# Kernel tuning notes

Hardware: AMD Instinct MI355X
Metric: run time of the kernel (lower is better)

The kernel has to match this reference:

```python
import jax, jax.numpy as jnp
import numpy as np

N_NODES = 100000
N_EDGES = 1600000
IN_DIM, HID_DIM, OUT_DIM = 128, 64, 64


def _graph_conv(src, dst, h, W, b, n_nodes):
    # DGL GraphConv, norm='both': out = D_in^{-1/2} A (D_out^{-1/2} h W) + b
    ones = jnp.ones(src.shape[0], dtype=h.dtype)
    deg_out = jax.ops.segment_sum(ones, src, num_segments=n_nodes)
    deg_in = jax.ops.segment_sum(ones, dst, num_segments=n_nodes)
    norm_src = jax.lax.rsqrt(jnp.maximum(deg_out, 1.0))  # [N]
    norm_dst = jax.lax.rsqrt(jnp.maximum(deg_in, 1.0))   # [N]
    # project first (in_dim >= out_dim path), then aggregate over edges
    x = (h * norm_src[:, None]) @ W                      # [N, d_out]
    msg = x[src]                                         # [E, d_out] gather
    agg = jax.ops.segment_sum(msg, dst, num_segments=n_nodes)  # [N, d_out]
    return agg * norm_dst[:, None] + b


def setup_inputs() -> dict:
    key = jax.random.key(0)
    k = jax.random.split(key, 6)
    h = jax.random.normal(k[0], (N_NODES, IN_DIM), dtype=jnp.float32)
    src = jax.random.randint(k[1], (N_EDGES,), 0, N_NODES, dtype=jnp.int32)
    dst = jax.random.randint(k[2], (N_EDGES,), 0, N_NODES, dtype=jnp.int32)
    W1 = jax.random.normal(k[3], (IN_DIM, HID_DIM), dtype=jnp.float32) / np.sqrt(IN_DIM)
    b1 = jnp.zeros((HID_DIM,), dtype=jnp.float32)
    W2 = jax.random.normal(k[4], (HID_DIM, OUT_DIM), dtype=jnp.float32) / np.sqrt(HID_DIM)
    b2 = jnp.zeros((OUT_DIM,), dtype=jnp.float32)
    return {"h": h, "src": src, "dst": dst, "W1": W1, "b1": b1, "W2": W2, "b2": b2}


def reference(h, src, dst, W1, b1, W2, b2):
    x = _graph_conv(src, dst, h, W1, b1, N_NODES)
    x = jax.nn.elu(x)  # act = nn.ELU()
    x = _graph_conv(src, dst, x, W2, b2, N_NODES)
    return x  # last_act is None
```

## Files before the change

### kernel.cpp

```cpp
#include <hip/hip_runtime.h>
#include <math.h>

#define CH 4096
#define NBUK_MAX 256
#define MAXB 12288
#define SRC_BITS 17

typedef short bf16x8 __attribute__((ext_vector_type(8)));
typedef float f32x4 __attribute__((ext_vector_type(4)));
typedef float f32x2 __attribute__((ext_vector_type(2)));

__device__ __forceinline__ unsigned short f2bf(float f) {
    union { float f; unsigned int u; } v; v.f = f;
    unsigned int r = (v.u + 0x7FFFu + ((v.u >> 16) & 1u)) >> 16;
    return (unsigned short)r;
}
__device__ __forceinline__ float bf2f(unsigned short u) {
    union { unsigned int u; float f; } v; v.u = ((unsigned int)u) << 16;
    return v.f;
}
__device__ __forceinline__ float bflo(unsigned int u) {
    union { unsigned int u; float f; } v; v.u = u << 16;
    return v.f;
}
__device__ __forceinline__ float bfhi(unsigned int u) {
    union { unsigned int u; float f; } v; v.u = u & 0xFFFF0000u;
    return v.f;
}

__global__ __launch_bounds__(256) void p1a_kernel(const int* __restrict__ src, const int* __restrict__ dst,
                                                  int* __restrict__ mat, int E, int B1, int nbuk) {
    __shared__ int hd[NBUK_MAX], hs[NBUK_MAX];
    const int t = threadIdx.x;
    if (t < nbuk) { hd[t] = 0; hs[t] = 0; }
    __syncthreads();
    const int base = blockIdx.x * CH;
    const int cnt = min(CH, E - base);
    for (int k = t; k < cnt; k += 256) {
        int d = dst[base + k];
        int s = src[base + k];
        atomicAdd(&hd[d >> 9], 1);
        atomicAdd(&hs[s >> 9], 1);
    }
    __syncthreads();
    if (t < nbuk) {
        mat[t * B1 + blockIdx.x] = hd[t];
        mat[(nbuk + t) * B1 + blockIdx.x] = hs[t];
    }
}

__global__ __launch_bounds__(256) void scan1_kernel(const int* __restrict__ cnt,
                                                    int* __restrict__ seg,
                                                    int* __restrict__ bsums, int N) {
    __shared__ int tsum[256];
    const int t = threadIdx.x;
    const int base = blockIdx.x * 1024 + t * 4;
    int v0 = (base + 0 < N) ? cnt[base + 0] : 0;
    int v1 = (base + 1 < N) ? cnt[base + 1] : 0;
    int v2 = (base + 2 < N) ? cnt[base + 2] : 0;
    int v3 = (base + 3 < N) ? cnt[base + 3] : 0;
    tsum[t] = v0 + v1 + v2 + v3;
    __syncthreads();
    for (int off = 1; off < 256; off <<= 1) {
        int x = (t >= off) ? tsum[t - off] : 0;
        __syncthreads();
        if (t >= off) tsum[t] += x;
        __syncthreads();
    }
    int run = (t > 0) ? tsum[t - 1] : 0;
    if (base + 0 < N) seg[base + 0] = run; run += v0;
    if (base + 1 < N) seg[base + 1] = run; run += v1;
    if (base + 2 < N) seg[base + 2] = run; run += v2;
    if (base + 3 < N) seg[base + 3] = run;
    if (t == 255) bsums[blockIdx.x] = tsum[255];
}

__global__ void scan2_kernel(int* __restrict__ bsums, int* __restrict__ seg, int N, int G) {
    __shared__ int s[256];
    int t = threadIdx.x;
    if (t < G) s[t] = bsums[t];
    __syncthreads();
    if (t == 0) {
        int run = 0;
        for (int i = 0; i < G; ++i) { int v = s[i]; s[i] = run; run += v; }
        seg[N] = run;
    }
    __syncthreads();
    if (t < G) bsums[t] = s[t];
}

__global__ __launch_bounds__(256) void scan3_kernel(int* __restrict__ seg,
                                                    const int* __restrict__ bsums, int N) {
    int add = bsums[blockIdx.x];
    int base = blockIdx.x * 1024 + threadIdx.x * 4;
#pragma unroll
    for (int i = 0; i < 4; ++i) {
        int idx = base + i;
        if (idx < N) seg[idx] += add;
    }
}

__global__ __launch_bounds__(256) void p1c_kernel(const int* __restrict__ src, const int* __restrict__ dst,
                                                  const int* __restrict__ mat,
                                                  const int* __restrict__ scan,
                                                  int* __restrict__ pedge,
                                                  int E, int B1, int nbuk) {
    __shared__ int hd[NBUK_MAX], hs[NBUK_MAX];
    __shared__ int curD[NBUK_MAX], curS[NBUK_MAX];
    __shared__ int baseD[NBUK_MAX], baseS[NBUK_MAX];
    __shared__ int stD[CH];
    __shared__ int stS[CH];
    const int t = threadIdx.x;
    if (t < nbuk) {
        hd[t] = mat[t * B1 + blockIdx.x];
        hs[t] = mat[(nbuk + t) * B1 + blockIdx.x];
    }
    const int base = blockIdx.x * CH;
    const int cnt = min(CH, E - base);
    int dl[CH / 256], sl[CH / 256];
#pragma unroll
    for (int k = 0; k < CH / 256; ++k) {
        int i = t + k * 256;
        if (i < cnt) {
            dl[k] = dst[base + i];
            sl[k] = src[base + i];
        }
    }
    __syncthreads();
    for (int off = 1; off < nbuk; off <<= 1) {
        int v0 = (t >= off && t < nbuk) ? hd[t - off] : 0;
        int w0 = (t >= off && t < nbuk) ? hs[t - off] : 0;
        __syncthreads();
        if (t < nbuk) { hd[t] += v0; hs[t] += w0; }
        __syncthreads();
    }
    if (t < nbuk) {
        int excD = t ? hd[t - 1] : 0;
        int excS = t ? hs[t - 1] : 0;
        curD[t] = excD;
        curS[t] = excS;
        baseD[t] = scan[t * B1 + blockIdx.x] - excD;
        baseS[t] = scan[(nbuk + t) * B1 + blockIdx.x] - excS;
    }
    __syncthreads();
#pragma unroll
    for (int k = 0; k < CH / 256; ++k) {
        int i = t + k * 256;
        if (i < cnt) {
            int j = dl[k] >> 9;
            int p = atomicAdd(&curD[j], 1);
            stD[p] = ((dl[k] & 511) << SRC_BITS) | sl[k];
            int jq = sl[k] >> 9;
            int q = atomicAdd(&curS[jq], 1);
            stS[q] = sl[k];
        }
    }
    __syncthreads();
    for (int i = t; i < cnt; i += 256) {
        int lo = 0, hi = nbuk - 1;
        while (lo < hi) { int mid = (lo + hi) >> 1; if (hd[mid] > i) hi = mid; else lo = mid + 1; }
        pedge[baseD[lo] + i] = stD[i];
        int lo2 = 0, hi2 = nbuk - 1;
        while (lo2 < hi2) { int mid = (lo2 + hi2) >> 1; if (hs[mid] > i) hi2 = mid; else lo2 = mid + 1; }
        pedge[baseS[lo2] + i] = stS[i];
    }
}

__global__ __launch_bounds__(512) void p2s2_kernel(const int* __restrict__ pedge,
                                                   const int* __restrict__ scan,
                                                   int* __restrict__ esrc, int* __restrict__ seg,
                                                   float* __restrict__ norm_dst,
                                                   float* __restrict__ norm_src,
                                                   int N, int E, int B1, int nbuk) {
    __shared__ int h[512];
    __shared__ int cur[512];
    __shared__ int stage[MAXB];
    const int t = threadIdx.x;
    const int b0 = blockIdx.x;
    if (b0 >= nbuk) {
        const int b = b0 - nbuk;
        h[t] = 0;
        __syncthreads();
        const int sb0 = scan[(nbuk + b) * B1];
        const int sb1 = scan[(nbuk + b + 1) * B1];
        for (int i = sb0 + t; i < sb1; i += 512) atomicAdd(&h[pedge[i] & 511], 1);
        __syncthreads();
        int n = (b << 9) + t;
        if (n < N) norm_src[n] = rsqrtf(fmaxf((float)h[t], 1.0f));
        return;
    }
    const int b = b0;
    h[t] = 0;
    __syncthreads();
    const int bb0 = scan[b * B1];
    const int bb1 = scan[(b + 1) * B1];
    for (int i = bb0 + t; i < bb1; i += 512) atomicAdd(&h[(pedge[i] >> SRC_BITS) & 511], 1);
    __syncthreads();
    for (int off = 1; off < 512; off <<= 1) {
        int v = (t >= off) ? h[t - off] : 0;
        __syncthreads();
        h[t] += v;
        __syncthreads();
    }
    {
        int exc = t ? h[t - 1] : 0;
        cur[t] = exc;
        int n = (b << 9) + t;
        if (n < N) {
            seg[n] = bb0 + exc;
            norm_dst[n] = rsqrtf(fmaxf((float)(h[t] - exc), 1.0f));
        }
        if (b == 0 && t == 0) seg[N] = E;
    }
    __syncthreads();
    const int cnt = bb1 - bb0;
    for (int i = bb0 + t; i < bb1; i += 512) {
        int v = pedge[i];
        int j = (v >> SRC_BITS) & 511;
        int p = atomicAdd(&cur[j], 1);
        int s = v & ((1 << SRC_BITS) - 1);
        if (p < MAXB) stage[p] = s; else esrc[bb0 + p] = s;
    }
    __syncthreads();
    for (int i = t; i < cnt && i < MAXB; i += 512) esrc[bb0 + i] = stage[i];
}

template<int K>
__global__ __launch_bounds__(256) void gemm_norm(const float* __restrict__ H,
                                                 const float* __restrict__ W,
                                                 const float* __restrict__ norm,
                                                 unsigned short* __restrict__ X, int N) {
    constexpr int KP = K + 8;
    __shared__ __align__(16) unsigned short sHi[64 * KP];
    __shared__ __align__(16) unsigned short sLo[64 * KP];
    const int tid = threadIdx.x;

    for (int idx = tid; idx < K * 64; idx += 256) {
        int k = idx >> 6;
        int c = idx & 63;
        float v = W[idx];
        unsigned short hi = f2bf(v);
        sHi[c * KP + k] = hi;
        sLo[c * KP + k] = f2bf(v - bf2f(hi));
    }
    __syncthreads();

    const int w = tid >> 6;
    const int lane = tid & 63;
    const int quad = lane >> 4;
    const int l16 = lane & 15;
    const int n0 = blockIdx.x * 64;
    const int arow = n0 + w * 16 + l16;
    const int arow_c = (arow < N) ? arow : (N - 1);
    const float* Hrow = H + (size_t)arow_c * K + quad * 8;

    f32x4 acc[4];
#pragma unroll
    for (int t = 0; t < 4; ++t) acc[t] = (f32x4){0.0f, 0.0f, 0.0f, 0.0f};

    float4 p0 = *(const float4*)(Hrow + 0);
    float4 p1 = *(const float4*)(Hrow + 4);

#pragma unroll
    for (int kc = 0; kc < K / 32; ++kc) {
        const float v[8] = {p0.x, p0.y, p0.z, p0.w, p1.x, p1.y, p1.z, p1.w};
        bf16x8 aHi, aLo;
#pragma unroll
        for (int j = 0; j < 8; ++j) {
            unsigned short hi = f2bf(v[j]);
            aHi[j] = (short)hi;
            aLo[j] = (short)f2bf(v[j] - bf2f(hi));
        }
        if (kc + 1 < K / 32) {
            p0 = *(const float4*)(Hrow + (kc + 1) * 32 + 0);
            p1 = *(const float4*)(Hrow + (kc + 1) * 32 + 4);
        }
        const int kbase = kc * 32 + quad * 8;
#pragma unroll
        for (int t = 0; t < 4; ++t) {
            const int col = t * 16 + l16;
            const bf16x8 bHi = *(const bf16x8*)&sHi[col * KP + kbase];
            const bf16x8 bLo = *(const bf16x8*)&sLo[col * KP + kbase];
            acc[t] = __builtin_amdgcn_mfma_f32_16x16x32_bf16(aLo, bHi, acc[t], 0, 0, 0);
            acc[t] = __builtin_amdgcn_mfma_f32_16x16x32_bf16(aHi, bLo, acc[t], 0, 0, 0);
            acc[t] = __builtin_amdgcn_mfma_f32_16x16x32_bf16(aHi, bHi, acc[t], 0, 0, 0);
        }
    }

#pragma unroll
    for (int r = 0; r < 4; ++r) {
        const int node = n0 + w * 16 + quad * 4 + r;
        if (node < N) {
            const float s = norm[node];
#pragma unroll
            for (int t = 0; t < 4; ++t) {
                X[(size_t)node * 64 + t * 16 + l16] = f2bf(acc[t][r] * s);
            }
        } else if (node == N) {
#pragma unroll
            for (int t = 0; t < 4; ++t) {
                X[(size_t)node * 64 + t * 16 + l16] = 0;
            }
        }
    }
}

template<bool ELU>
__global__ __launch_bounds__(256) void segsum_kernel(const unsigned short* __restrict__ X,
                                                     const int* __restrict__ esrc,
                                                     const int* __restrict__ seg,
                                                     const float* __restrict__ norm_dst,
                                                     const float* __restrict__ bias,
                                                     float* __restrict__ out, int N) {
    const int node = blockIdx.x * 4 + (threadIdx.x >> 6);
    const int lane = threadIdx.x & 63;
    if (node >= N) return;
    const int eh = lane >> 4;
    const int fl = lane & 15;
    const int s0 = seg[node];
    const int s1 = seg[node + 1];
    const unsigned short* Xf = X + fl * 4;
    f32x2 A0 = {0.0f, 0.0f};
    f32x2 A1 = {0.0f, 0.0f};
    int e = s0;
    for (; e + 16 <= s1; e += 16) {
        const int base = e + eh * 4;
        const int r0 = esrc[base + 0];
        const int r1 = esrc[base + 1];
        const int r2 = esrc[base + 2];
        const int r3 = esrc[base + 3];
        const uint2 u0 = *(const uint2*)&Xf[(size_t)r0 * 64];
        const uint2 u1 = *(const uint2*)&Xf[(size_t)r1 * 64];
        const uint2 u2 = *(const uint2*)&Xf[(size_t)r2 * 64];
        const uint2 u3 = *(const uint2*)&Xf[(size_t)r3 * 64];
        A0 += (f32x2){bflo(u0.x), bfhi(u0.x)}; A1 += (f32x2){bflo(u0.y), bfhi(u0.y)};
        A0 += (f32x2){bflo(u1.x), bfhi(u1.x)}; A1 += (f32x2){bflo(u1.y), bfhi(u1.y)};
        A0 += (f32x2){bflo(u2.x), bfhi(u2.x)}; A1 += (f32x2){bflo(u2.y), bfhi(u2.y)};
        A0 += (f32x2){bflo(u3.x), bfhi(u3.x)}; A1 += (f32x2){bflo(u3.y), bfhi(u3.y)};
    }
    if (e < s1) {
        const int base = e + eh * 4;
        const int i0 = esrc[base + 0];
        const int i1 = esrc[base + 1];
        const int i2 = esrc[base + 2];
        const int i3 = esrc[base + 3];
        const int r0 = (base + 0 < s1) ? i0 : N;
        const int r1 = (base + 1 < s1) ? i1 : N;
        const int r2 = (base + 2 < s1) ? i2 : N;
        const int r3 = (base + 3 < s1) ? i3 : N;
        const uint2 u0 = *(const uint2*)&Xf[(size_t)r0 * 64];
        const uint2 u1 = *(const uint2*)&Xf[(size_t)r1 * 64];
        const uint2 u2 = *(const uint2*)&Xf[(size_t)r2 * 64];
        const uint2 u3 = *(const uint2*)&Xf[(size_t)r3 * 64];
        A0 += (f32x2){bflo(u0.x), bfhi(u0.x)}; A1 += (f32x2){bflo(u0.y), bfhi(u0.y)};
        A0 += (f32x2){bflo(u1.x), bfhi(u1.x)}; A1 += (f32x2){bflo(u1.y), bfhi(u1.y)};
        A0 += (f32x2){bflo(u2.x), bfhi(u2.x)}; A1 += (f32x2){bflo(u2.y), bfhi(u2.y)};
        A0 += (f32x2){bflo(u3.x), bfhi(u3.x)}; A1 += (f32x2){bflo(u3.y), bfhi(u3.y)};
    }
    float a0 = A0.x, a1 = A0.y, a2 = A1.x, a3 = A1.y;
    a0 += __shfl(a0, lane ^ 16); a1 += __shfl(a1, lane ^ 16);
    a2 += __shfl(a2, lane ^ 16); a3 += __shfl(a3, lane ^ 16);
    a0 += __shfl(a0, lane ^ 32); a1 += __shfl(a1, lane ^ 32);
    a2 += __shfl(a2, lane ^ 32); a3 += __shfl(a3, lane ^ 32);
    if (eh == 0) {
        const float s = norm_dst[node];
        const float4 bb = *(const float4*)&bias[fl * 4];
        float4 r;
        r.x = a0 * s + bb.x;
        r.y = a1 * s + bb.y;
        r.z = a2 * s + bb.z;
        r.w = a3 * s + bb.w;
        if (ELU) {
            r.x = r.x > 0.0f ? r.x : expm1f(r.x);
            r.y = r.y > 0.0f ? r.y : expm1f(r.y);
            r.z = r.z > 0.0f ? r.z : expm1f(r.z);
            r.w = r.w > 0.0f ? r.w : expm1f(r.w);
        }
        *(float4*)&out[(size_t)node * 64 + fl * 4] = r;
    }
}

extern "C" void kernel_launch(void* const* d_in, const int* in_sizes, int n_in,
                              void* d_out, int out_size, void* d_ws, size_t ws_size,
                              hipStream_t stream) {
    const float* h   = (const float*)d_in[0];
    const int*   src = (const int*)d_in[1];
    const int*   dst = (const int*)d_in[2];
    const float* W1  = (const float*)d_in[3];
    const float* b1  = (const float*)d_in[4];
    const float* W2  = (const float*)d_in[5];
    const float* b2  = (const float*)d_in[6];
    float* out = (float*)d_out;

    const int N = in_sizes[0] / 128;
    const int E = in_sizes[1];
    const int nbuk = (N + 511) >> 9;
    const int B1 = (E + CH - 1) / CH;
    const int M = 2 * nbuk * B1;

    int* iw = (int*)d_ws;
    int* mat   = iw;
    int* scanb = mat + M;
    int* bsums = scanb + M + 4;
    int* pedge = bsums + 256;
    int* esrc  = pedge + 2 * (size_t)E;
    int* seg   = esrc + (size_t)E + 16;
    float* fw       = (float*)(seg + (size_t)N + 4);
    float* norm_src = fw;
    float* norm_dst = fw + (size_t)N;
    float* H1       = fw + 2 * (size_t)N;
    unsigned short* Xb = (unsigned short*)(H1 + 64 * (size_t)N);

    p1a_kernel<<<B1, 256, 0, stream>>>(src, dst, mat, E, B1, nbuk);
    const int G = (M + 1023) / 1024;
    scan1_kernel<<<G, 256, 0, stream>>>(mat, scanb, bsums, M);
    scan2_kernel<<<1, 256, 0, stream>>>(bsums, scanb, M, G);
    scan3_kernel<<<G, 256, 0, stream>>>(scanb, bsums, M);
    p1c_kernel<<<B1, 256, 0, stream>>>(src, dst, mat, scanb, pedge, E, B1, nbuk);
    p2s2_kernel<<<2 * nbuk, 512, 0, stream>>>(pedge, scanb, esrc, seg, norm_dst, norm_src,
                                              N, E, B1, nbuk);

    const int segGrid = (N + 3) / 4;

    gemm_norm<128><<<(N + 63) / 64, 256, 0, stream>>>(h, W1, norm_src, Xb, N);
    segsum_kernel<true><<<segGrid, 256, 0, stream>>>(Xb, esrc, seg, norm_dst, b1, H1, N);

    gemm_norm<64><<<(N + 63) / 64, 256, 0, stream>>>(H1, W2, norm_src, Xb, N);
    segsum_kernel<false><<<segGrid, 256, 0, stream>>>(Xb, esrc, seg, norm_dst, b2, out, N);
}
```

Baseline: 291.1 us.

## Compute source degrees with global atomics and widen segsum gathers to 16B

The source-side bucket sort is dropped. Out-degrees are now counted with global atomics on a zeroed deg array, and a small kernel turns them into norm_src. This halves the pedge traffic and the sorting work in p1c and p2. The segsum kernel now gathers each neighbour row with one 16-byte load per lane over 8 edge groups, and uses a butterfly shuffle transpose-reduce so each lane writes one output feature. The gemm grid is extended so the padding row N is zeroed. The risks are atomic contention on deg and more shuffle/select work.

```diff
diff --git a/kernel.cpp b/kernel.cpp
--- a/kernel.cpp
+++ b/kernel.cpp
@@ -29,10 +29,11 @@
 }
 
 __global__ __launch_bounds__(256) void p1a_kernel(const int* __restrict__ src, const int* __restrict__ dst,
-                                                  int* __restrict__ mat, int E, int B1, int nbuk) {
-    __shared__ int hd[NBUK_MAX], hs[NBUK_MAX];
+                                                  int* __restrict__ mat, int* __restrict__ deg,
+                                                  int E, int B1, int nbuk) {
+    __shared__ int hd[NBUK_MAX];
     const int t = threadIdx.x;
-    if (t < nbuk) { hd[t] = 0; hs[t] = 0; }
+    if (t < nbuk) hd[t] = 0;
     __syncthreads();
     const int base = blockIdx.x * CH;
     const int cnt = min(CH, E - base);
@@ -40,13 +41,16 @@
         int d = dst[base + k];
         int s = src[base + k];
         atomicAdd(&hd[d >> 9], 1);
-        atomicAdd(&hs[s >> 9], 1);
-    }
-    __syncthreads();
-    if (t < nbuk) {
-        mat[t * B1 + blockIdx.x] = hd[t];
-        mat[(nbuk + t) * B1 + blockIdx.x] = hs[t];
-    }
+        atomicAdd(&deg[s], 1);
+    }
+    __syncthreads();
+    if (t < nbuk) mat[t * B1 + blockIdx.x] = hd[t];
+}
+
+__global__ __launch_bounds__(256) void norm_src_kernel(const int* __restrict__ deg,
+                                                       float* __restrict__ ns, int N) {
+    int i = blockIdx.x * 256 + threadIdx.x;
+    if (i < N) ns[i] = rsqrtf(fmaxf((float)deg[i], 1.0f));
 }
 
 __global__ __launch_bounds__(256) void scan1_kernel(const int* __restrict__ cnt,
@@ -105,16 +109,12 @@
                                                   const int* __restrict__ scan,
                                                   int* __restrict__ pedge,
                                                   int E, int B1, int nbuk) {
-    __shared__ int hd[NBUK_MAX], hs[NBUK_MAX];
-    __shared__ int curD[NBUK_MAX], curS[NBUK_MAX];
-    __shared__ int baseD[NBUK_MAX], baseS[NBUK_MAX];
+    __shared__ int hd[NBUK_MAX];
+    __shared__ int curD[NBUK_MAX];
+    __shared__ int baseD[NBUK_MAX];
     __shared__ int stD[CH];
-    __shared__ int stS[CH];
     const int t = threadIdx.x;
-    if (t < nbuk) {
-        hd[t] = mat[t * B1 + blockIdx.x];
-        hs[t] = mat[(nbuk + t) * B1 + blockIdx.x];
-    }
+    if (t < nbuk) hd[t] = mat[t * B1 + blockIdx.x];
     const int base = blockIdx.x * CH;
     const int cnt = min(CH, E - base);
     int dl[CH / 256], sl[CH / 256];
@@ -129,18 +129,14 @@
     __syncthreads();
     for (int off = 1; off < nbuk; off <<= 1) {
         int v0 = (t >= off && t < nbuk) ? hd[t - off] : 0;
-        int w0 = (t >= off && t < nbuk) ? hs[t - off] : 0;
-        __syncthreads();
-        if (t < nbuk) { hd[t] += v0; hs[t] += w0; }
+        __syncthreads();
+        if (t < nbuk) hd[t] += v0;
         __syncthreads();
     }
     if (t < nbuk) {
         int excD = t ? hd[t - 1] : 0;
-        int excS = t ? hs[t - 1] : 0;
         curD[t] = excD;
-        curS[t] = excS;
         baseD[t] = scan[t * B1 + blockIdx.x] - excD;
-        baseS[t] = scan[(nbuk + t) * B1 + blockIdx.x] - excS;
     }
     __syncthreads();
 #pragma unroll
@@ -150,9 +146,6 @@
             int j = dl[k] >> 9;
             int p = atomicAdd(&curD[j], 1);
             stD[p] = ((dl[k] & 511) << SRC_BITS) | sl[k];
-            int jq = sl[k] >> 9;
-            int q = atomicAdd(&curS[jq], 1);
-            stS[q] = sl[k];
         }
     }
     __syncthreads();
@@ -160,36 +153,19 @@
         int lo = 0, hi = nbuk - 1;
         while (lo < hi) { int mid = (lo + hi) >> 1; if (hd[mid] > i) hi = mid; else lo = mid + 1; }
         pedge[baseD[lo] + i] = stD[i];
-        int lo2 = 0, hi2 = nbuk - 1;
-        while (lo2 < hi2) { int mid = (lo2 + hi2) >> 1; if (hs[mid] > i) hi2 = mid; else lo2 = mid + 1; }
-        pedge[baseS[lo2] + i] = stS[i];
-    }
-}
-
-__global__ __launch_bounds__(512) void p2s2_kernel(const int* __restrict__ pedge,
-                                                   const int* __restrict__ scan,
-                                                   int* __restrict__ esrc, int* __restrict__ seg,
-                                                   float* __restrict__ norm_dst,
-                                                   float* __restrict__ norm_src,
-                                                   int N, int E, int B1, int nbuk) {
+    }
+}
+
+__global__ __launch_bounds__(512) void p2_kernel(const int* __restrict__ pedge,
+                                                 const int* __restrict__ scan,
+                                                 int* __restrict__ esrc, int* __restrict__ seg,
+                                                 float* __restrict__ norm_dst,
+                                                 int N, int E, int B1) {
     __shared__ int h[512];
     __shared__ int cur[512];
     __shared__ int stage[MAXB];
     const int t = threadIdx.x;
-    const int b0 = blockIdx.x;
-    if (b0 >= nbuk) {
-        const int b = b0 - nbuk;
-        h[t] = 0;
-        __syncthreads();
-        const int sb0 = scan[(nbuk + b) * B1];
-        const int sb1 = scan[(nbuk + b + 1) * B1];
-        for (int i = sb0 + t; i < sb1; i += 512) atomicAdd(&h[pedge[i] & 511], 1);
-        __syncthreads();
-        int n = (b << 9) + t;
-        if (n < N) norm_src[n] = rsqrtf(fmaxf((float)h[t], 1.0f));
-        return;
-    }
-    const int b = b0;
+    const int b = blockIdx.x;
     h[t] = 0;
     __syncthreads();
     const int bb0 = scan[b * B1];
@@ -312,72 +288,75 @@
                                                      const float* __restrict__ norm_dst,
                                                      const float* __restrict__ bias,
                                                      float* __restrict__ out, int N) {
-    const int node = blockIdx.x * 4 + (threadIdx.x >> 6);
+    const int node = __builtin_amdgcn_readfirstlane(blockIdx.x * 4 + (threadIdx.x >> 6));
+    if (node >= N) return;
     const int lane = threadIdx.x & 63;
-    if (node >= N) return;
-    const int eh = lane >> 4;
-    const int fl = lane & 15;
+    const int eh = lane >> 3;
+    const int fl = lane & 7;
+    const unsigned flo = (unsigned)fl << 4;
+    const int fown = fl * 8 + ((eh & 1) << 2) + (eh & 2) + (eh >> 2);
+    const float bv = bias[fown];
     const int s0 = seg[node];
     const int s1 = seg[node + 1];
-    const unsigned short* Xf = X + fl * 4;
-    f32x2 A0 = {0.0f, 0.0f};
-    f32x2 A1 = {0.0f, 0.0f};
+    const char* Xb = (const char*)X;
+    f32x2 A0 = {0.0f, 0.0f}, A1 = {0.0f, 0.0f}, A2 = {0.0f, 0.0f}, A3 = {0.0f, 0.0f};
+#define ACC8(u) \
+    A0 += (f32x2){bflo(u.x), bfhi(u.x)}; A1 += (f32x2){bflo(u.y), bfhi(u.y)}; \
+    A2 += (f32x2){bflo(u.z), bfhi(u.z)}; A3 += (f32x2){bflo(u.w), bfhi(u.w)};
     int e = s0;
     for (; e + 16 <= s1; e += 16) {
-        const int base = e + eh * 4;
-        const int r0 = esrc[base + 0];
-        const int r1 = esrc[base + 1];
-        const int r2 = esrc[base + 2];
-        const int r3 = esrc[base + 3];
-        const uint2 u0 = *(const uint2*)&Xf[(size_t)r0 * 64];
-        const uint2 u1 = *(const uint2*)&Xf[(size_t)r1 * 64];
-        const uint2 u2 = *(const uint2*)&Xf[(size_t)r2 * 64];
-        const uint2 u3 = *(const uint2*)&Xf[(size_t)r3 * 64];
-        A0 += (f32x2){bflo(u0.x), bfhi(u0.x)}; A1 += (f32x2){bflo(u0.y), bfhi(u0.y)};
-        A0 += (f32x2){bflo(u1.x), bfhi(u1.x)}; A1 += (f32x2){bflo(u1.y), bfhi(u1.y)};
-        A0 += (f32x2){bflo(u2.x), bfhi(u2.x)}; A1 += (f32x2){bflo(u2.y), bfhi(u2.y)};
-        A0 += (f32x2){bflo(u3.x), bfhi(u3.x)}; A1 += (f32x2){bflo(u3.y), bfhi(u3.y)};
+        const int r0 = esrc[e + eh];
+        const int r1 = esrc[e + 8 + eh];
+        const uint4 u0 = *(const uint4*)(Xb + ((((unsigned)r0) << 7) | flo));
+        const uint4 u1 = *(const uint4*)(Xb + ((((unsigned)r1) << 7) | flo));
+        ACC8(u0);
+        ACC8(u1);
     }
     if (e < s1) {
-        const int base = e + eh * 4;
-        const int i0 = esrc[base + 0];
-        const int i1 = esrc[base + 1];
-        const int i2 = esrc[base + 2];
-        const int i3 = esrc[base + 3];
-        const int r0 = (base + 0 < s1) ? i0 : N;
-        const int r1 = (base + 1 < s1) ? i1 : N;
-        const int r2 = (base + 2 < s1) ? i2 : N;
-        const int r3 = (base + 3 < s1) ? i3 : N;
-        const uint2 u0 = *(const uint2*)&Xf[(size_t)r0 * 64];
-        const uint2 u1 = *(const uint2*)&Xf[(size_t)r1 * 64];
-        const uint2 u2 = *(const uint2*)&Xf[(size_t)r2 * 64];
-        const uint2 u3 = *(const uint2*)&Xf[(size_t)r3 * 64];
-        A0 += (f32x2){bflo(u0.x), bfhi(u0.x)}; A1 += (f32x2){bflo(u0.y), bfhi(u0.y)};
-        A0 += (f32x2){bflo(u1.x), bfhi(u1.x)}; A1 += (f32x2){bflo(u1.y), bfhi(u1.y)};
-        A0 += (f32x2){bflo(u2.x), bfhi(u2.x)}; A1 += (f32x2){bflo(u2.y), bfhi(u2.y)};
-        A0 += (f32x2){bflo(u3.x), bfhi(u3.x)}; A1 += (f32x2){bflo(u3.y), bfhi(u3.y)};
-    }
+        const int i0 = e + eh;
+        const int i1 = e + 8 + eh;
+        const int q0 = esrc[i0];
+        const int q1 = esrc[i1];
+        const int r0 = (i0 < s1) ? q0 : N;
+        const int r1 = (i1 < s1) ? q1 : N;
+        const uint4 u0 = *(const uint4*)(Xb + ((((unsigned)r0) << 7) | flo));
+        const uint4 u1 = *(const uint4*)(Xb + ((((unsigned)r1) << 7) | flo));
+        ACC8(u0);
+        ACC8(u1);
+    }
+#undef ACC8
     float a0 = A0.x, a1 = A0.y, a2 = A1.x, a3 = A1.y;
-    a0 += __shfl(a0, lane ^ 16); a1 += __shfl(a1, lane ^ 16);
-    a2 += __shfl(a2, lane ^ 16); a3 += __shfl(a3, lane ^ 16);
-    a0 += __shfl(a0, lane ^ 32); a1 += __shfl(a1, lane ^ 32);
-    a2 += __shfl(a2, lane ^ 32); a3 += __shfl(a3, lane ^ 32);
-    if (eh == 0) {
-        const float s = norm_dst[node];
-        const float4 bb = *(const float4*)&bias[fl * 4];
-        float4 r;
-        r.x = a0 * s + bb.x;
-        r.y = a1 * s + bb.y;
-        r.z = a2 * s + bb.z;
-        r.w = a3 * s + bb.w;
-        if (ELU) {
-            r.x = r.x > 0.0f ? r.x : expm1f(r.x);
-            r.y = r.y > 0.0f ? r.y : expm1f(r.y);
-            r.z = r.z > 0.0f ? r.z : expm1f(r.z);
-            r.w = r.w > 0.0f ? r.w : expm1f(r.w);
-        }
-        *(float4*)&out[(size_t)node * 64 + fl * 4] = r;
-    }
+    float a4 = A2.x, a5 = A2.y, a6 = A3.x, a7 = A3.y;
+    const bool p0 = (eh & 1) != 0;
+    const bool p1 = (eh & 2) != 0;
+    const bool p2 = (eh & 4) != 0;
+    float t0, t1, t2, t3;
+    {
+        float sA = p0 ? a0 : a4, kA = p0 ? a4 : a0;
+        float sB = p0 ? a1 : a5, kB = p0 ? a5 : a1;
+        float sC = p0 ? a2 : a6, kC = p0 ? a6 : a2;
+        float sD = p0 ? a3 : a7, kD = p0 ? a7 : a3;
+        t0 = kA + __shfl_xor(sA, 8);
+        t1 = kB + __shfl_xor(sB, 8);
+        t2 = kC + __shfl_xor(sC, 8);
+        t3 = kD + __shfl_xor(sD, 8);
+    }
+    float u0, u1;
+    {
+        float sA = p1 ? t0 : t2, kA = p1 ? t2 : t0;
+        float sB = p1 ? t1 : t3, kB = p1 ? t3 : t1;
+        u0 = kA + __shfl_xor(sA, 16);
+        u1 = kB + __shfl_xor(sB, 16);
+    }
+    float v;
+    {
+        float sA = p2 ? u0 : u1, kA = p2 ? u1 : u0;
+        v = kA + __shfl_xor(sA, 32);
+    }
+    const float s = norm_dst[node];
+    float r = v * s + bv;
+    if (ELU) r = r > 0.0f ? r : expm1f(r);
+    out[(size_t)node * 64 + fown] = r;
 }
 
 extern "C" void kernel_launch(void* const* d_in, const int* in_sizes, int n_in,
@@ -396,35 +375,39 @@
     const int E = in_sizes[1];
     const int nbuk = (N + 511) >> 9;
     const int B1 = (E + CH - 1) / CH;
-    const int M = 2 * nbuk * B1;
+    const int M = nbuk * B1;
 
     int* iw = (int*)d_ws;
     int* mat   = iw;
     int* scanb = mat + M;
     int* bsums = scanb + M + 4;
-    int* pedge = bsums + 256;
-    int* esrc  = pedge + 2 * (size_t)E;
+    int* deg   = bsums + 256;
+    int* pedge = deg + N;
+    int* esrc  = pedge + (size_t)E;
     int* seg   = esrc + (size_t)E + 16;
-    float* fw       = (float*)(seg + (size_t)N + 4);
-    float* norm_src = fw;
-    float* norm_dst = fw + (size_t)N;
-    float* H1       = fw + 2 * (size_t)N;
+    uintptr_t fp = (uintptr_t)(seg + (size_t)N + 4);
+    fp = (fp + 63) & ~(uintptr_t)63;
+    float* norm_src = (float*)fp;
+    float* norm_dst = norm_src + (size_t)N;
+    float* H1       = norm_dst + (size_t)N;
     unsigned short* Xb = (unsigned short*)(H1 + 64 * (size_t)N);
 
-    p1a_kernel<<<B1, 256, 0, stream>>>(src, dst, mat, E, B1, nbuk);
+    hipMemsetAsync(deg, 0, (size_t)N * sizeof(int), stream);
+    p1a_kernel<<<B1, 256, 0, stream>>>(src, dst, mat, deg, E, B1, nbuk);
+    norm_src_kernel<<<(N + 255) / 256, 256, 0, stream>>>(deg, norm_src, N);
     const int G = (M + 1023) / 1024;
     scan1_kernel<<<G, 256, 0, stream>>>(mat, scanb, bsums, M);
     scan2_kernel<<<1, 256, 0, stream>>>(bsums, scanb, M, G);
     scan3_kernel<<<G, 256, 0, stream>>>(scanb, bsums, M);
     p1c_kernel<<<B1, 256, 0, stream>>>(src, dst, mat, scanb, pedge, E, B1, nbuk);
-    p2s2_kernel<<<2 * nbuk, 512, 0, stream>>>(pedge, scanb, esrc, seg, norm_dst, norm_src,
-                                              N, E, B1, nbuk);
+    p2_kernel<<<nbuk, 512, 0, stream>>>(pedge, scanb, esrc, seg, norm_dst, N, E, B1);
 
     const int segGrid = (N + 3) / 4;
-
-    gemm_norm<128><<<(N + 63) / 64, 256, 0, stream>>>(h, W1, norm_src, Xb, N);
+    const int gemmGrid = (N + 64) / 64;
+
+    gemm_norm<128><<<gemmGrid, 256, 0, stream>>>(h, W1, norm_src, Xb, N);
     segsum_kernel<true><<<segGrid, 256, 0, stream>>>(Xb, esrc, seg, norm_dst, b1, H1, N);
 
-    gemm_norm<64><<<(N + 63) / 64, 256, 0, stream>>>(H1, W2, norm_src, Xb, N);
+    gemm_norm<64><<<gemmGrid, 256, 0, stream>>>(H1, W2, norm_src, Xb, N);
     segsum_kernel<false><<<segGrid, 256, 0, stream>>>(Xb, esrc, seg, norm_dst, b2, out, N);
 }
```

Result: slower. 335.4 us (+15.2%).
